# Optimization experiments

Hardware: AMD Instinct MI355X
Metric: run time of the kernel (lower is better)

The kernel has to match this reference:

```python
import jax, jax.numpy as jnp
import numpy as np

WS = (5, 8, 8)   # window_size (Wz, Wh, Ww)
SS = (2, 4, 4)   # shift_size  (Sz, Sh, Sw)
EPS = 1e-5


def _rel_pos_index(ws):
    Wz, Wh, Ww = ws
    coords = np.stack(np.meshgrid(np.arange(Wz), np.arange(Wh), np.arange(Ww), indexing='ij'))
    cf = coords.reshape(3, -1)                      # (3, N)
    rel = cf[:, :, None] - cf[:, None, :]           # (3, N, N)
    rel = rel.transpose(1, 2, 0).astype(np.int64)   # (N, N, 3)
    rel[..., 0] += Wz - 1
    rel[..., 1] += Wh - 1
    rel[..., 2] += Ww - 1
    rel[..., 0] *= (2 * Wh - 1) * (2 * Ww - 1)
    rel[..., 1] *= (2 * Ww - 1)
    return rel.sum(-1)                              # (N, N)


def _shift_mask(Z, H, W, ws, ss):
    Wz, Wh, Ww = ws
    Sz, Sh, Sw = ss
    img = np.zeros((Z, H, W), dtype=np.float32)
    cnt = 0
    for zs in (slice(0, -Wz), slice(-Wz, -Sz), slice(-Sz, None)):
        for hs in (slice(0, -Wh), slice(-Wh, -Sh), slice(-Sh, None)):
            for wl in (slice(0, -Ww), slice(-Ww, -Sw), slice(-Sw, None)):
                img[zs, hs, wl] = cnt
                cnt += 1
    mw = img.reshape(Z // Wz, Wz, H // Wh, Wh, W // Ww, Ww)
    mw = mw.transpose(0, 2, 4, 1, 3, 5).reshape(-1, Wz * Wh * Ww)  # (nW, N)
    diff = mw[:, None, :] - mw[:, :, None]                          # (nW, N, N)
    return np.where(diff != 0, np.float32(-100.0), np.float32(0.0))


def _layernorm(x, g, b):
    mu = jnp.mean(x, axis=-1, keepdims=True)
    var = jnp.var(x, axis=-1, keepdims=True)
    return (x - mu) * jax.lax.rsqrt(var + EPS) * g + b


def setup_inputs() -> dict:
    key = jax.random.key(0)
    ks = jax.random.split(key, 6)
    B, C, Z, H, W = 2, 192, 10, 48, 48
    nH = 6
    hidden = 4 * C
    tbl = (2 * WS[0] - 1) * (2 * WS[1] - 1) * (2 * WS[2] - 1)
    return {
        'x': jax.random.normal(ks[0], (B, C, Z, H, W), jnp.float32),
        'norm1_g': jnp.ones((C,), jnp.float32),
        'norm1_b': jnp.zeros((C,), jnp.float32),
        'qkv_w': jax.random.normal(ks[1], (3 * C, C), jnp.float32) * 0.02,
        'qkv_b': jnp.zeros((3 * C,), jnp.float32),
        'proj_w': jax.random.normal(ks[2], (C, C), jnp.float32) * 0.02,
        'proj_b': jnp.zeros((C,), jnp.float32),
        'rpb_table': jax.random.normal(ks[3], (tbl, nH), jnp.float32) * 0.02,
        'norm2_g': jnp.ones((C,), jnp.float32),
        'norm2_b': jnp.zeros((C,), jnp.float32),
        'fc1_w': jax.random.normal(ks[4], (hidden, C), jnp.float32) * 0.02,
        'fc1_b': jnp.zeros((hidden,), jnp.float32),
        'fc2_w': jax.random.normal(ks[5], (C, hidden), jnp.float32) * 0.02,
        'fc2_b': jnp.zeros((C,), jnp.float32),
    }


def reference(x, norm1_g, norm1_b, qkv_w, qkv_b, proj_w, proj_b, rpb_table,
              norm2_g, norm2_b, fc1_w, fc1_b, fc2_w, fc2_b):
    B, C, Z, H, W = x.shape
    Wz, Wh, Ww = WS
    Sz, Sh, Sw = SS
    nH = rpb_table.shape[1]
    hd = C // nH
    N = Wz * Wh * Ww
    scale = hd ** -0.5

    h = jnp.transpose(x, (0, 2, 3, 4, 1))            # (B,Z,H,W,C) channels-last
    shortcut = h
    h = _layernorm(h, norm1_g, norm1_b)
    # cyclic shift
    h = jnp.roll(h, shift=(-Sz, -Sh, -Sw), axis=(1, 2, 3))
    # window partition -> (BW, N, C)
    win = h.reshape(B, Z // Wz, Wz, H // Wh, Wh, W // Ww, Ww, C)
    win = win.transpose(0, 1, 3, 5, 2, 4, 6, 7).reshape(-1, N, C)
    BW = win.shape[0]

    qkv = win @ qkv_w.T + qkv_b                      # (BW, N, 3C)
    qkv = qkv.reshape(BW, N, 3, nH, hd)
    q = jnp.transpose(qkv[:, :, 0], (0, 2, 1, 3)) * scale   # (BW,nH,N,hd)
    k = jnp.transpose(qkv[:, :, 1], (0, 2, 1, 3))
    v = jnp.transpose(qkv[:, :, 2], (0, 2, 1, 3))

    attn = jnp.einsum('bhnd,bhmd->bhnm', q, k)       # (BW,nH,N,N)
    idx = _rel_pos_index(WS)                          # static (N,N)
    bias = rpb_table[idx.reshape(-1)].reshape(N, N, nH)
    attn = attn + jnp.transpose(bias, (2, 0, 1))[None]

    mask = jnp.asarray(_shift_mask(Z, H, W, WS, SS)) # (nW,N,N), static
    nW = mask.shape[0]
    attn = attn.reshape(B, nW, nH, N, N) + mask[None, :, None]
    attn = jax.nn.softmax(attn.reshape(BW, nH, N, N), axis=-1)

    out = jnp.einsum('bhnm,bhmd->bhnd', attn, v)     # (BW,nH,N,hd)
    out = jnp.transpose(out, (0, 2, 1, 3)).reshape(BW, N, C)
    out = out @ proj_w.T + proj_b

    # window reverse -> (B,Z,H,W,C)
    out = out.reshape(B, Z // Wz, H // Wh, W // Ww, Wz, Wh, Ww, C)
    out = out.transpose(0, 1, 4, 2, 5, 3, 6, 7).reshape(B, Z, H, W, C)
    out = jnp.roll(out, shift=(Sz, Sh, Sw), axis=(1, 2, 3))

    h = shortcut + out
    h2 = _layernorm(h, norm2_g, norm2_b)
    h2 = jax.nn.gelu(h2 @ fc1_w.T + fc1_b, approximate=False)
    h2 = h2 @ fc2_w.T + fc2_b
    h = h + h2
    return jnp.transpose(h, (0, 4, 1, 2, 3))          # back to (B,C,Z,H,W)
```

## Files before the change

kernel.cpp:

```cpp
#include <hip/hip_runtime.h>
#include <hip/hip_bf16.h>

typedef __hip_bfloat16 bf16;
typedef __attribute__((ext_vector_type(4))) float f32x4;
typedef __attribute__((ext_vector_type(8))) short bf16x8;
typedef __attribute__((ext_vector_type(4))) short bf16x4;
typedef __attribute__((ext_vector_type(4))) int i32x4;

#define DEVINL __device__ __forceinline__

constexpr int SPB = 23040;
constexpr int TOK = 46080;
constexpr int NWT = 320;
constexpr int NHEAD = 6;
constexpr int HD = 32;
constexpr int HID = 768;
constexpr int TBL = 2025;
constexpr float SCALE = 0.17677669529663687f;

DEVINL float b2f(bf16 v) { return __bfloat162float(v); }
DEVINL float bflo(unsigned u) { unsigned w = u << 16; return __builtin_bit_cast(float, w); }

DEVINL unsigned cvtpk(float a, float b) {
  unsigned r;
  asm("v_cvt_pk_bf16_f32 %0, %1, %2" : "=v"(r) : "v"(a), "v"(b));
  return r;
}

DEVINL f32x4 mfma16(bf16x4 a, bf16x4 b, f32x4 c) {
#if __has_builtin(__builtin_amdgcn_mfma_f32_16x16x16bf16_1k)
  return __builtin_amdgcn_mfma_f32_16x16x16bf16_1k(a, b, c, 0, 0, 0);
#elif __has_builtin(__builtin_amdgcn_mfma_f32_16x16x16_bf16)
  return __builtin_amdgcn_mfma_f32_16x16x16_bf16(a, b, c, 0, 0, 0);
#else
  f32x4 d;
  asm volatile("v_mfma_f32_16x16x16_bf16 %0, %1, %2, %3\n\ts_nop 7\n\ts_nop 7"
               : "=v"(d) : "v"(a), "v"(b), "v"(c));
  return d;
#endif
}

DEVINL void gload16(const bf16* g, bf16* l) {
  __builtin_amdgcn_global_load_lds(
      (const __attribute__((address_space(1))) void*)g,
      (__attribute__((address_space(3))) void*)l, 16, 0, 0);
}

__global__ void k_flag(const unsigned* __restrict__ g1, int* __restrict__ flag) {
  if (threadIdx.x == 0) flag[0] = (g1[0] == 0x3F800000u) ? 1 : 0;
}

struct CvtArgs {
  const void* src[13];
  bf16* dst[13];
  int n[13];
};

__global__ __launch_bounds__(256) void k_cvt(CvtArgs a, const int* __restrict__ flag) {
  int bi = blockIdx.y;
  int n = a.n[bi];
  bool f32m = flag[0] != 0;
  const float* sf = (const float*)a.src[bi];
  const bf16* sh = (const bf16*)a.src[bi];
  bf16* d = a.dst[bi];
  if (f32m) {
    for (int i = blockIdx.x * 256 + threadIdx.x; i < n; i += gridDim.x * 256)
      d[i] = __float2bfloat16(sf[i]);
  } else {
    for (int i = blockIdx.x * 256 + threadIdx.x; i < n; i += gridDim.x * 256)
      d[i] = sh[i];
  }
}

__global__ __launch_bounds__(256) void k_ln1win(
    const void* __restrict__ xv, const bf16* __restrict__ g, const bf16* __restrict__ be,
    const int* __restrict__ flag, float* __restrict__ hbuf, bf16* __restrict__ win) {
  __shared__ float tile[192][64];
  __shared__ float red[2][4][64];
  __shared__ float stat[2][64];
  int t = threadIdx.x;
  int p = t & 63, q = t >> 6;
  int base = blockIdx.x * 64;
  int b = base / SPB, s0 = base % SPB;
  bool f32m = flag[0] != 0;
  float sum = 0.f, sq = 0.f;
  if (f32m) {
    const float* x = (const float*)xv;
    for (int c = q; c < 192; c += 4) {
      float v = x[(long)(b * 192 + c) * SPB + s0 + p];
      tile[c][p] = v; sum += v; sq += v * v;
    }
  } else {
    const bf16* x = (const bf16*)xv;
    for (int c = q; c < 192; c += 4) {
      float v = b2f(x[(long)(b * 192 + c) * SPB + s0 + p]);
      tile[c][p] = v; sum += v; sq += v * v;
    }
  }
  red[0][q][p] = sum; red[1][q][p] = sq;
  __syncthreads();
  if (t < 64) {
    float s1 = red[0][0][t] + red[0][1][t] + red[0][2][t] + red[0][3][t];
    float s2 = red[1][0][t] + red[1][1][t] + red[1][2][t] + red[1][3][t];
    float mu = s1 * (1.f / 192.f);
    float var = s2 * (1.f / 192.f) - mu * mu;
    stat[0][t] = mu;
    stat[1][t] = rsqrtf(var + 1e-5f);
  }
  __syncthreads();
  int p2 = t >> 2, quad = t & 3;
  int spos = s0 + p2;
  int z = spos / 2304, rm = spos % 2304;
  int hh = rm / 48, ww = rm % 48;
  int zr = z - 2; if (zr < 0) zr += 10;
  int hr = hh - 4; if (hr < 0) hr += 48;
  int wr = ww - 4; if (wr < 0) wr += 48;
  int zw = zr / 5, zi = zr - zw * 5;
  int hw = hr >> 3, hi = hr & 7;
  int wv = wr >> 3, wi = wr & 7;
  int wb = ((b * 2 + zw) * 6 + hw) * 6 + wv;
  int n = (zi * 8 + hi) * 8 + wi;
  float mu = stat[0][p2], rs = stat[1][p2];
  long hb = (long)(b * SPB + spos) * 192;
  long wbse = (long)(wb * NWT + n) * 192;
  for (int c = quad * 48; c < quad * 48 + 48; ++c) {
    float v = tile[c][p2];
    hbuf[hb + c] = v;
    win[wbse + c] = __float2bfloat16((v - mu) * rs * b2f(g[c]) + b2f(be[c]));
  }
}

template <int EPI, int NN>
__global__ __launch_bounds__(256, 5) void k_gemm(
    const bf16* __restrict__ A, const bf16* __restrict__ Wt, const bf16* __restrict__ bias,
    int K, bf16* __restrict__ out0, float* __restrict__ hbuf, void* __restrict__ outb,
    const int* __restrict__ flag) {
  __shared__ __align__(16) char smem[24576];
  bf16* As = (bf16*)smem;
  bf16* Bs = (bf16*)(smem + 16384);

  int t = threadIdx.x;
  constexpr int NBLK = 360 * NN;
  int wg = (blockIdx.x & 7) * (NBLK / 8) + (blockIdx.x >> 3);
  int m0 = (wg / NN) * 128, n0 = (wg % NN) * 64;
  int wave = t >> 6, lane = t & 63;
  int lr = lane & 15, lg = lane >> 4;
  int wbase = t & ~63;
  f32x4 acc[2][4];
#pragma unroll
  for (int a = 0; a < 2; ++a)
#pragma unroll
    for (int bb2 = 0; bb2 < 4; ++bb2) acc[a][bb2] = (f32x4){0.f, 0.f, 0.f, 0.f};

  for (int kc = 0; kc < K; kc += 64) {
#pragma unroll
    for (int it = 0; it < 4; ++it) {
      int s = it * 256 + t;
      int r = s >> 3, c = s & 7;
      int cg = c ^ (r & 7);
      gload16(&A[(long)(m0 + r) * K + kc + cg * 8], As + (it * 256 + wbase) * 8);
    }
#pragma unroll
    for (int it = 0; it < 2; ++it) {
      int s = it * 256 + t;
      int r = s >> 3, c = s & 7;
      int cg = c ^ (r & 7);
      gload16(&Wt[(long)(n0 + r) * K + kc + cg * 8], Bs + (it * 256 + wbase) * 8);
    }
    __syncthreads();
#pragma unroll
    for (int ks = 0; ks < 2; ++ks) {
      int ra = wave * 32 + lr;
      bf16x8 a0 = *(const bf16x8*)(As + ra * 64 + (((ks * 4 + lg) ^ (ra & 7)) * 8));
      bf16x8 a1 = *(const bf16x8*)(As + (ra + 16) * 64 + (((ks * 4 + lg) ^ ((ra + 16) & 7)) * 8));
#pragma unroll
      for (int nn = 0; nn < 4; ++nn) {
        int rb = nn * 16 + lr;
        bf16x8 bfr = *(const bf16x8*)(Bs + rb * 64 + (((ks * 4 + lg) ^ (rb & 7)) * 8));
        acc[0][nn] = __builtin_amdgcn_mfma_f32_16x16x32_bf16(a0, bfr, acc[0][nn], 0, 0, 0);
        acc[1][nn] = __builtin_amdgcn_mfma_f32_16x16x32_bf16(a1, bfr, acc[1][nn], 0, 0, 0);
      }
    }
    __syncthreads();
  }

  if constexpr (EPI == 0) {
    bf16* Ct = (bf16*)smem;
#pragma unroll
    for (int nn = 0; nn < 4; ++nn) {
      int f = n0 + nn * 16 + lr;
      float bv = b2f(bias[f]);
      float sc = (f < 192) ? SCALE : 1.f;
#pragma unroll
      for (int mi = 0; mi < 2; ++mi)
#pragma unroll
        for (int r = 0; r < 4; ++r) {
          int rl = wave * 32 + mi * 16 + lg * 4 + r;
          Ct[rl * 72 + nn * 16 + lr] = __float2bfloat16((acc[mi][nn][r] + bv) * sc);
        }
    }
    __syncthreads();
#pragma unroll
    for (int it = 0; it < 4; ++it) {
      int fi = it * 256 + t;
      int row = fi >> 3, c8 = (fi & 7) * 8;
      int f0 = n0 + c8;
      int plane = f0 >> 5, d0 = f0 & 31;
      long dst = ((long)plane * TOK + m0 + row) * 32 + d0;
      *(i32x4*)&out0[dst] = *(const i32x4*)&Ct[row * 72 + c8];
    }
  } else if constexpr (EPI == 1) {
    float* Cf = (float*)smem;
#pragma unroll
    for (int half = 0; half < 2; ++half) {
      if ((wave >> 1) == half) {
#pragma unroll
        for (int nn = 0; nn < 4; ++nn) {
          int c = n0 + nn * 16 + lr;
          float bv = b2f(bias[c]);
#pragma unroll
          for (int mi = 0; mi < 2; ++mi)
#pragma unroll
            for (int r = 0; r < 4; ++r) {
              int rl = wave * 32 + mi * 16 + lg * 4 + r - half * 64;
              Cf[rl * 68 + nn * 16 + lr] = acc[mi][nn][r] + bv;
            }
        }
      }
      __syncthreads();
#pragma unroll
      for (int it = 0; it < 4; ++it) {
        int fi = it * 256 + t;
        int row = fi >> 4, c4 = (fi & 15) * 4;
        int grow = m0 + half * 64 + row;
        int wb = grow / NWT, i = grow % NWT;
        int b = wb / 72, wIdx = wb % 72;
        int zw = wIdx / 36, hw = (wIdx % 36) / 6, wv = wIdx % 6;
        int zi = i >> 6, hi = (i >> 3) & 7, wi = i & 7;
        int zf = zw * 5 + zi + 2; if (zf >= 10) zf -= 10;
        int hf = hw * 8 + hi + 4; if (hf >= 48) hf -= 48;
        int wf = wv * 8 + wi + 4; if (wf >= 48) wf -= 48;
        long hb = (long)(b * SPB + zf * 2304 + hf * 48 + wf) * 192 + n0 + c4;
        f32x4 cur = *(f32x4*)&hbuf[hb];
        cur += *(const f32x4*)&Cf[row * 68 + c4];
        *(f32x4*)&hbuf[hb] = cur;
      }
      __syncthreads();
    }
  } else if constexpr (EPI == 2) {
    bf16* Ct = (bf16*)smem;
#pragma unroll
    for (int nn = 0; nn < 4; ++nn) {
      int f = n0 + nn * 16 + lr;
      float bv = b2f(bias[f]);
#pragma unroll
      for (int mi = 0; mi < 2; ++mi)
#pragma unroll
        for (int r = 0; r < 4; ++r) {
          int rl = wave * 32 + mi * 16 + lg * 4 + r;
          float v = acc[mi][nn][r] + bv;
          v = 0.5f * v * (1.f + erff(v * 0.70710678118654752f));
          Ct[rl * 72 + nn * 16 + lr] = __float2bfloat16(v);
        }
    }
    __syncthreads();
#pragma unroll
    for (int it = 0; it < 4; ++it) {
      int fi = it * 256 + t;
      int row = fi >> 3, c8 = (fi & 7) * 8;
      long dst = (long)(m0 + row) * HID + n0 + c8;
      *(i32x4*)&out0[dst] = *(const i32x4*)&Ct[row * 72 + c8];
    }
  } else {
    float* eld = (float*)smem;
    int b = m0 / SPB, sbase = m0 % SPB;
    bool f32m = flag[0] != 0;
#pragma unroll
    for (int half = 0; half < 2; ++half) {
      if ((wave >> 1) == half) {
#pragma unroll
        for (int nn = 0; nn < 4; ++nn) {
          int c = n0 + nn * 16 + lr;
          float bv = b2f(bias[c]);
#pragma unroll
          for (int mi = 0; mi < 2; ++mi)
#pragma unroll
            for (int r = 0; r < 4; ++r) {
              int rl = wave * 32 + mi * 16 + lg * 4 + r;
              int row = m0 + rl;
              float v = acc[mi][nn][r] + bv + hbuf[(long)row * 192 + c];
              eld[(rl - half * 64) * 65 + nn * 16 + lr] = v;
            }
        }
      }
      __syncthreads();
      int cl = t >> 2, sq = t & 3;
      long ob = (long)(b * 192 + n0 + cl) * SPB + sbase + half * 64;
      if (f32m) {
        float* ob32 = (float*)outb;
#pragma unroll
        for (int k2 = 0; k2 < 16; ++k2) {
          int sl = sq * 16 + k2;
          ob32[ob + sl] = eld[sl * 65 + cl];
        }
      } else {
        bf16* ob16 = (bf16*)outb;
#pragma unroll
        for (int k2 = 0; k2 < 16; ++k2) {
          int sl = sq * 16 + k2;
          ob16[ob + sl] = __float2bfloat16(eld[sl * 65 + cl]);
        }
      }
      __syncthreads();
    }
  }
}

__global__ __launch_bounds__(256, 3) void k_attn_mfma(
    const bf16* __restrict__ qkv, const bf16* __restrict__ rpb, bf16* __restrict__ o) {
  __shared__ __align__(16) bf16 KlA[320 * 32];
  __shared__ __align__(16) bf16 QlA[320 * 32];
  __shared__ __align__(16) bf16 Vt[32][328];
  __shared__ unsigned short bias_l[2032];
  __shared__ unsigned short info[320];

  int t = threadIdx.x;
  int blk = blockIdx.x;
  int head = blk % NHEAD, wb = blk / NHEAD;
  const bf16* qp = qkv + ((long)head * TOK + wb * NWT) * HD;
  const bf16* kp = qkv + ((long)(6 + head) * TOK + wb * NWT) * HD;
  const bf16* vp = qkv + ((long)(12 + head) * TOK + wb * NWT) * HD;
  int wIdx = wb % 72;
  int wz = wIdx / 36, hw = (wIdx % 36) / 6, wv = wIdx % 6;
  int wbase = t & ~63;

#pragma unroll
  for (int it = 0; it < 5; ++it) {
    int s = it * 256 + t;
    int row = s >> 2, c = s & 3;
    int cg = c ^ (row & 3);
    gload16(&kp[row * 32 + cg * 8], KlA + (it * 256 + wbase) * 8);
    gload16(&qp[row * 32 + cg * 8], QlA + (it * 256 + wbase) * 8);
  }
#pragma unroll
  for (int it = 0; it < 3; ++it) {
    int idx = t + 256 * it;
    if (idx < 640) {
      int kp2 = idx % 160, c8 = idx / 160;
      i32x4 va = *(const i32x4*)&vp[(kp2 * 2) * HD + c8 * 8];
      i32x4 vb = *(const i32x4*)&vp[(kp2 * 2 + 1) * HD + c8 * 8];
#pragma unroll
      for (int e = 0; e < 8; ++e) {
        unsigned lo = ((unsigned)va[e >> 1] >> ((e & 1) * 16)) & 0xffffu;
        unsigned hi = ((unsigned)vb[e >> 1] >> ((e & 1) * 16)) & 0xffffu;
        *(unsigned*)&Vt[c8 * 8 + e][kp2 * 2] = lo | (hi << 16);
      }
    }
  }
  for (int idx = t; idx < TBL; idx += 256)
    bias_l[idx] = ((const unsigned short*)rpb)[idx * NHEAD + head];
  for (int idx = t; idx < NWT; idx += 256) {
    int zi = idx >> 6, hi2 = (idx >> 3) & 7, wi = idx & 7;
    int zr = wz * 5 + zi, hr = hw * 8 + hi2, wr = wv * 8 + wi;
    int rid = (zr < 5 ? 0 : (zr < 8 ? 9 : 18)) + (hr < 40 ? 0 : (hr < 44 ? 3 : 6)) +
              (wr < 40 ? 0 : (wr < 44 ? 1 : 2));
    info[idx] = (unsigned short)(((zi * 225 + hi2 * 15 + wi) << 5) | rid);
  }
  __syncthreads();

  int wave = t >> 6, lane = t & 63;
  int lr = lane & 15, lg = lane >> 4;

  unsigned cj01[20], cj23[20];
#pragma unroll
  for (int tt = 0; tt < 20; ++tt) {
    int k0 = tt * 16 + lg * 4;
    cj01[tt] = *(const unsigned*)&info[k0];
    cj23[tt] = *(const unsigned*)&info[k0 + 2];
  }

  int csw = (lg ^ (lr & 3)) * 8;

  for (int qi = 0; qi < 5; ++qi) {
    int qbl = qi * 64 + wave * 16;
    bf16x8 qf = *(const bf16x8*)(QlA + (qbl + lr) * 32 + csw);
    f32x4 sc[20];
#pragma unroll
    for (int tt = 0; tt < 20; ++tt) {
      bf16x8 kf = *(const bf16x8*)(KlA + (tt * 16 + lr) * 32 + csw);
      sc[tt] = __builtin_amdgcn_mfma_f32_16x16x32_bf16(kf, qf, (f32x4){0.f, 0.f, 0.f, 0.f}, 0, 0, 0);
    }
    unsigned ciq = info[qbl + lr];
    int ci1012 = (int)(ciq >> 5) + 1012;
    float mxv = -1e30f;
#pragma unroll
    for (int tt = 0; tt < 20; ++tt) {
      unsigned w0 = cj01[tt], w1 = cj23[tt];
      unsigned kin0 = w0 & 0xffffu, kin1 = w0 >> 16;
      unsigned kin2 = w1 & 0xffffu, kin3 = w1 >> 16;
      float s0 = sc[tt][0] + bflo((unsigned)bias_l[ci1012 - (int)(kin0 >> 5)]);
      float s1 = sc[tt][1] + bflo((unsigned)bias_l[ci1012 - (int)(kin1 >> 5)]);
      float s2 = sc[tt][2] + bflo((unsigned)bias_l[ci1012 - (int)(kin2 >> 5)]);
      float s3 = sc[tt][3] + bflo((unsigned)bias_l[ci1012 - (int)(kin3 >> 5)]);
      if ((kin0 ^ ciq) & 31u) s0 -= 100.f;
      if ((kin1 ^ ciq) & 31u) s1 -= 100.f;
      if ((kin2 ^ ciq) & 31u) s2 -= 100.f;
      if ((kin3 ^ ciq) & 31u) s3 -= 100.f;
      sc[tt][0] = s0; sc[tt][1] = s1; sc[tt][2] = s2; sc[tt][3] = s3;
      mxv = fmaxf(mxv, fmaxf(fmaxf(s0, s1), fmaxf(s2, s3)));
    }
    mxv = fmaxf(mxv, __shfl_xor(mxv, 16));
    mxv = fmaxf(mxv, __shfl_xor(mxv, 32));
    float sum = 0.f;
#pragma unroll
    for (int tt = 0; tt < 20; ++tt) {
      float p0 = __expf(sc[tt][0] - mxv);
      float p1 = __expf(sc[tt][1] - mxv);
      float p2 = __expf(sc[tt][2] - mxv);
      float p3 = __expf(sc[tt][3] - mxv);
      sc[tt][0] = p0; sc[tt][1] = p1; sc[tt][2] = p2; sc[tt][3] = p3;
      sum += (p0 + p1) + (p2 + p3);
    }
    sum += __shfl_xor(sum, 16);
    sum += __shfl_xor(sum, 32);
    float rl = 1.f / sum;

    f32x4 oacc0 = {0.f, 0.f, 0.f, 0.f}, oacc1 = {0.f, 0.f, 0.f, 0.f};
#pragma unroll
    for (int tt = 0; tt < 20; ++tt) {
      unsigned pk0 = cvtpk(sc[tt][0], sc[tt][1]);
      unsigned pk1 = cvtpk(sc[tt][2], sc[tt][3]);
      union { unsigned u[2]; bf16x4 v; } pu;
      pu.u[0] = pk0; pu.u[1] = pk1;
      bf16x4 v0 = *(const bf16x4*)&Vt[lr][tt * 16 + lg * 4];
      bf16x4 v1 = *(const bf16x4*)&Vt[16 + lr][tt * 16 + lg * 4];
      oacc0 = mfma16(pu.v, v0, oacc0);
      oacc1 = mfma16(pu.v, v1, oacc1);
    }
    int rli = __builtin_bit_cast(int, rl);
    float rl4[4];
#pragma unroll
    for (int r = 0; r < 4; ++r)
      rl4[r] = __builtin_bit_cast(float, __builtin_amdgcn_ds_bpermute((lg * 4 + r) * 4, rli));
#pragma unroll
    for (int r = 0; r < 4; ++r) {
      bf16* pr = o + ((long)(wb * NWT) + qbl + lg * 4 + r) * 192 + head * 32;
      pr[lr] = __float2bfloat16(oacc0[r] * rl4[r]);
      pr[16 + lr] = __float2bfloat16(oacc1[r] * rl4[r]);
    }
  }
}

__global__ __launch_bounds__(256) void k_ln2(
    const float* __restrict__ h, const bf16* __restrict__ g, const bf16* __restrict__ be,
    bf16* __restrict__ o) {
  int wave = threadIdx.x >> 6, lane = threadIdx.x & 63;
  float g0 = b2f(g[lane]), g1 = b2f(g[lane + 64]), g2 = b2f(g[lane + 128]);
  float b0 = b2f(be[lane]), b1 = b2f(be[lane + 64]), b2v = b2f(be[lane + 128]);
  for (long row = (long)blockIdx.x * 4 + wave; row < TOK; row += (long)gridDim.x * 4) {
    const float* hr = h + row * 192;
    float v0 = hr[lane], v1 = hr[lane + 64], v2 = hr[lane + 128];
    float s1 = v0 + v1 + v2;
    float s2 = v0 * v0 + v1 * v1 + v2 * v2;
#pragma unroll
    for (int off = 32; off > 0; off >>= 1) {
      s1 += __shfl_down(s1, off);
      s2 += __shfl_down(s2, off);
    }
    s1 = __shfl(s1, 0);
    s2 = __shfl(s2, 0);
    float mu = s1 * (1.f / 192.f);
    float rs = rsqrtf(s2 * (1.f / 192.f) - mu * mu + 1e-5f);
    bf16* orow = o + row * 192;
    orow[lane] = __float2bfloat16((v0 - mu) * rs * g0 + b0);
    orow[lane + 64] = __float2bfloat16((v1 - mu) * rs * g1 + b1);
    orow[lane + 128] = __float2bfloat16((v2 - mu) * rs * g2 + b2v);
  }
}

extern "C" void kernel_launch(void* const* d_in, const int* in_sizes, int n_in,
                              void* d_out, int out_size, void* d_ws, size_t ws_size,
                              hipStream_t stream) {
  (void)in_sizes; (void)n_in; (void)out_size; (void)ws_size;

  char* pp = (char*)d_ws;
  float* hbuf = (float*)pp;        pp += (size_t)TOK * 192 * 4;
  bf16* qkv   = (bf16*)pp;         pp += (size_t)3 * TOK * 192 * 2;
  bf16* win   = (bf16*)pp;         pp += (size_t)TOK * 192 * 2;
  bf16* fc1o  = (bf16*)pp;         pp += (size_t)TOK * HID * 2;
  int*  flag  = (int*)pp;          pp += 64;

  const int din_idx[13] = {1, 2, 3, 4, 5, 6, 7, 8, 9, 10, 11, 12, 13};
  const int sizes[13]   = {192, 192, 110592, 576, 36864, 192, 12150, 192, 192,
                           147456, 768, 147456, 192};
  bf16* canon[13];
  for (int ii = 0; ii < 13; ++ii) {
    canon[ii] = (bf16*)pp;
    size_t bytes = ((size_t)sizes[ii] * 2 + 63) & ~(size_t)63;
    pp += bytes;
  }
  bf16* n1g  = canon[0];
  bf16* n1b  = canon[1];
  bf16* qkvw = canon[2];
  bf16* qkvb = canon[3];
  bf16* projw= canon[4];
  bf16* projb= canon[5];
  bf16* rpb  = canon[6];
  bf16* n2g  = canon[7];
  bf16* n2b  = canon[8];
  bf16* fc1w = canon[9];
  bf16* fc1b = canon[10];
  bf16* fc2w = canon[11];
  bf16* fc2b = canon[12];

  CvtArgs ca;
  for (int ii = 0; ii < 13; ++ii) {
    ca.src[ii] = d_in[din_idx[ii]];
    ca.dst[ii] = canon[ii];
    ca.n[ii] = sizes[ii];
  }

  k_flag<<<1, 64, 0, stream>>>((const unsigned*)d_in[1], flag);
  k_cvt<<<dim3(64, 13), 256, 0, stream>>>(ca, flag);
  k_ln1win<<<TOK / 64, 256, 0, stream>>>(d_in[0], n1g, n1b, flag, hbuf, win);
  k_gemm<0, 9><<<360 * 9, 256, 0, stream>>>(win, qkvw, qkvb, 192, qkv, nullptr, nullptr, flag);
  k_attn_mfma<<<864, 256, 0, stream>>>(qkv, rpb, win);
  k_gemm<1, 3><<<360 * 3, 256, 0, stream>>>(win, projw, projb, 192, nullptr, hbuf, nullptr, flag);
  k_ln2<<<2048, 256, 0, stream>>>(hbuf, n2g, n2b, win);
  k_gemm<2, 12><<<360 * 12, 256, 0, stream>>>(win, fc1w, fc1b, 192, fc1o, nullptr, nullptr, flag);
  k_gemm<3, 3><<<360 * 3, 256, 0, stream>>>(fc1o, fc2w, fc2b, 768, nullptr, hbuf, d_out, flag);
}
```

Before: 255.6 us.

## Split attention softmax into two key phases to cut registers and LDS

```diff
diff --git a/kernel.cpp b/kernel.cpp
--- a/kernel.cpp
+++ b/kernel.cpp
@@ -316,10 +316,9 @@
   }
 }
 
-__global__ __launch_bounds__(256, 3) void k_attn_mfma(
+__global__ __launch_bounds__(256) void k_attn_mfma(
     const bf16* __restrict__ qkv, const bf16* __restrict__ rpb, bf16* __restrict__ o) {
   __shared__ __align__(16) bf16 KlA[320 * 32];
-  __shared__ __align__(16) bf16 QlA[320 * 32];
   __shared__ __align__(16) bf16 Vt[32][328];
   __shared__ unsigned short bias_l[2032];
   __shared__ unsigned short info[320];
@@ -340,7 +339,6 @@
     int row = s >> 2, c = s & 3;
     int cg = c ^ (row & 3);
     gload16(&kp[row * 32 + cg * 8], KlA + (it * 256 + wbase) * 8);
-    gload16(&qp[row * 32 + cg * 8], QlA + (it * 256 + wbase) * 8);
   }
 #pragma unroll
   for (int it = 0; it < 3; ++it) {
@@ -370,83 +368,91 @@
 
   int wave = t >> 6, lane = t & 63;
   int lr = lane & 15, lg = lane >> 4;
-
-  unsigned cj01[20], cj23[20];
-#pragma unroll
-  for (int tt = 0; tt < 20; ++tt) {
-    int k0 = tt * 16 + lg * 4;
-    cj01[tt] = *(const unsigned*)&info[k0];
-    cj23[tt] = *(const unsigned*)&info[k0 + 2];
-  }
-
   int csw = (lg ^ (lr & 3)) * 8;
 
   for (int qi = 0; qi < 5; ++qi) {
     int qbl = qi * 64 + wave * 16;
-    bf16x8 qf = *(const bf16x8*)(QlA + (qbl + lr) * 32 + csw);
-    f32x4 sc[20];
-#pragma unroll
-    for (int tt = 0; tt < 20; ++tt) {
-      bf16x8 kf = *(const bf16x8*)(KlA + (tt * 16 + lr) * 32 + csw);
-      sc[tt] = __builtin_amdgcn_mfma_f32_16x16x32_bf16(kf, qf, (f32x4){0.f, 0.f, 0.f, 0.f}, 0, 0, 0);
-    }
+    bf16x8 qf = *(const bf16x8*)&qp[(qbl + lr) * HD + lg * 8];
     unsigned ciq = info[qbl + lr];
     int ci1012 = (int)(ciq >> 5) + 1012;
-    float mxv = -1e30f;
-#pragma unroll
-    for (int tt = 0; tt < 20; ++tt) {
-      unsigned w0 = cj01[tt], w1 = cj23[tt];
-      unsigned kin0 = w0 & 0xffffu, kin1 = w0 >> 16;
-      unsigned kin2 = w1 & 0xffffu, kin3 = w1 >> 16;
-      float s0 = sc[tt][0] + bflo((unsigned)bias_l[ci1012 - (int)(kin0 >> 5)]);
-      float s1 = sc[tt][1] + bflo((unsigned)bias_l[ci1012 - (int)(kin1 >> 5)]);
-      float s2 = sc[tt][2] + bflo((unsigned)bias_l[ci1012 - (int)(kin2 >> 5)]);
-      float s3 = sc[tt][3] + bflo((unsigned)bias_l[ci1012 - (int)(kin3 >> 5)]);
-      if ((kin0 ^ ciq) & 31u) s0 -= 100.f;
-      if ((kin1 ^ ciq) & 31u) s1 -= 100.f;
-      if ((kin2 ^ ciq) & 31u) s2 -= 100.f;
-      if ((kin3 ^ ciq) & 31u) s3 -= 100.f;
-      sc[tt][0] = s0; sc[tt][1] = s1; sc[tt][2] = s2; sc[tt][3] = s3;
-      mxv = fmaxf(mxv, fmaxf(fmaxf(s0, s1), fmaxf(s2, s3)));
-    }
-    mxv = fmaxf(mxv, __shfl_xor(mxv, 16));
-    mxv = fmaxf(mxv, __shfl_xor(mxv, 32));
-    float sum = 0.f;
-#pragma unroll
-    for (int tt = 0; tt < 20; ++tt) {
-      float p0 = __expf(sc[tt][0] - mxv);
-      float p1 = __expf(sc[tt][1] - mxv);
-      float p2 = __expf(sc[tt][2] - mxv);
-      float p3 = __expf(sc[tt][3] - mxv);
-      sc[tt][0] = p0; sc[tt][1] = p1; sc[tt][2] = p2; sc[tt][3] = p3;
-      sum += (p0 + p1) + (p2 + p3);
-    }
-    sum += __shfl_xor(sum, 16);
-    sum += __shfl_xor(sum, 32);
-    float rl = 1.f / sum;
-
-    f32x4 oacc0 = {0.f, 0.f, 0.f, 0.f}, oacc1 = {0.f, 0.f, 0.f, 0.f};
-#pragma unroll
-    for (int tt = 0; tt < 20; ++tt) {
-      unsigned pk0 = cvtpk(sc[tt][0], sc[tt][1]);
-      unsigned pk1 = cvtpk(sc[tt][2], sc[tt][3]);
-      union { unsigned u[2]; bf16x4 v; } pu;
-      pu.u[0] = pk0; pu.u[1] = pk1;
-      bf16x4 v0 = *(const bf16x4*)&Vt[lr][tt * 16 + lg * 4];
-      bf16x4 v1 = *(const bf16x4*)&Vt[16 + lr][tt * 16 + lg * 4];
-      oacc0 = mfma16(pu.v, v0, oacc0);
-      oacc1 = mfma16(pu.v, v1, oacc1);
-    }
-    int rli = __builtin_bit_cast(int, rl);
-    float rl4[4];
-#pragma unroll
-    for (int r = 0; r < 4; ++r)
-      rl4[r] = __builtin_bit_cast(float, __builtin_amdgcn_ds_bpermute((lg * 4 + r) * 4, rli));
+
+    float mph0, sph0, mph1, sph1;
+    f32x4 oa00, oa01, oa10, oa11;
+
+#pragma unroll
+    for (int ph = 0; ph < 2; ++ph) {
+      f32x4 sc[10];
+#pragma unroll
+      for (int u = 0; u < 10; ++u) {
+        int tt = ph * 10 + u;
+        bf16x8 kf = *(const bf16x8*)(KlA + (tt * 16 + lr) * 32 + csw);
+        sc[u] = __builtin_amdgcn_mfma_f32_16x16x32_bf16(kf, qf, (f32x4){0.f, 0.f, 0.f, 0.f}, 0, 0, 0);
+      }
+      float mxv = -1e30f;
+#pragma unroll
+      for (int u = 0; u < 10; ++u) {
+        int tt = ph * 10 + u;
+        int k0 = tt * 16 + lg * 4;
+        unsigned w0 = *(const unsigned*)&info[k0];
+        unsigned w1 = *(const unsigned*)&info[k0 + 2];
+        unsigned kin0 = w0 & 0xffffu, kin1 = w0 >> 16;
+        unsigned kin2 = w1 & 0xffffu, kin3 = w1 >> 16;
+        float s0 = sc[u][0] + bflo((unsigned)bias_l[ci1012 - (int)(kin0 >> 5)]);
+        float s1 = sc[u][1] + bflo((unsigned)bias_l[ci1012 - (int)(kin1 >> 5)]);
+        float s2 = sc[u][2] + bflo((unsigned)bias_l[ci1012 - (int)(kin2 >> 5)]);
+        float s3 = sc[u][3] + bflo((unsigned)bias_l[ci1012 - (int)(kin3 >> 5)]);
+        if ((kin0 ^ ciq) & 31u) s0 -= 100.f;
+        if ((kin1 ^ ciq) & 31u) s1 -= 100.f;
+        if ((kin2 ^ ciq) & 31u) s2 -= 100.f;
+        if ((kin3 ^ ciq) & 31u) s3 -= 100.f;
+        sc[u][0] = s0; sc[u][1] = s1; sc[u][2] = s2; sc[u][3] = s3;
+        mxv = fmaxf(mxv, fmaxf(fmaxf(s0, s1), fmaxf(s2, s3)));
+      }
+      mxv = fmaxf(mxv, __shfl_xor(mxv, 16));
+      mxv = fmaxf(mxv, __shfl_xor(mxv, 32));
+      float sum = 0.f;
+#pragma unroll
+      for (int u = 0; u < 10; ++u) {
+        float p0 = __expf(sc[u][0] - mxv);
+        float p1 = __expf(sc[u][1] - mxv);
+        float p2 = __expf(sc[u][2] - mxv);
+        float p3 = __expf(sc[u][3] - mxv);
+        sc[u][0] = p0; sc[u][1] = p1; sc[u][2] = p2; sc[u][3] = p3;
+        sum += (p0 + p1) + (p2 + p3);
+      }
+      sum += __shfl_xor(sum, 16);
+      sum += __shfl_xor(sum, 32);
+
+      f32x4 o0 = {0.f, 0.f, 0.f, 0.f}, o1 = {0.f, 0.f, 0.f, 0.f};
+#pragma unroll
+      for (int u = 0; u < 10; ++u) {
+        int tt = ph * 10 + u;
+        unsigned pk0 = cvtpk(sc[u][0], sc[u][1]);
+        unsigned pk1 = cvtpk(sc[u][2], sc[u][3]);
+        union { unsigned uu[2]; bf16x4 v; } pu;
+        pu.uu[0] = pk0; pu.uu[1] = pk1;
+        bf16x4 v0 = *(const bf16x4*)&Vt[lr][tt * 16 + lg * 4];
+        bf16x4 v1 = *(const bf16x4*)&Vt[16 + lr][tt * 16 + lg * 4];
+        o0 = mfma16(pu.v, v0, o0);
+        o1 = mfma16(pu.v, v1, o1);
+      }
+      if (ph == 0) { mph0 = mxv; sph0 = sum; oa00 = o0; oa01 = o1; }
+      else         { mph1 = mxv; sph1 = sum; oa10 = o0; oa11 = o1; }
+    }
+
+    float m = fmaxf(mph0, mph1);
+    float f0 = __expf(mph0 - m), f1 = __expf(mph1 - m);
+    float rl = 1.f / (sph0 * f0 + sph1 * f1);
+    float a0 = f0 * rl, a1 = f1 * rl;
+    int a0i = __builtin_bit_cast(int, a0);
+    int a1i = __builtin_bit_cast(int, a1);
 #pragma unroll
     for (int r = 0; r < 4; ++r) {
+      float s0 = __builtin_bit_cast(float, __builtin_amdgcn_ds_bpermute((lg * 4 + r) * 4, a0i));
+      float s1 = __builtin_bit_cast(float, __builtin_amdgcn_ds_bpermute((lg * 4 + r) * 4, a1i));
       bf16* pr = o + ((long)(wb * NWT) + qbl + lg * 4 + r) * 192 + head * 32;
-      pr[lr] = __float2bfloat16(oacc0[r] * rl4[r]);
-      pr[16 + lr] = __float2bfloat16(oacc1[r] * rl4[r]);
+      pr[lr] = __float2bfloat16(oa00[r] * s0 + oa10[r] * s1);
+      pr[16 + lr] = __float2bfloat16(oa01[r] * s0 + oa11[r] * s1);
     }
   }
 }
```

Result: faster. 235.8 us (-7.8%).
